# Kernel tuning notes

Measured on AMD Instinct MI355X. Metric: run time of the kernel, lower is better.

## Reference

```python
import jax, jax.numpy as jnp
import numpy as np

D_MODEL = 1024
NHEAD = 16
D_HEAD = D_MODEL // NHEAD
D_FF = 2 * D_MODEL
EPS = 1e-5


def setup_inputs() -> dict:
    key = jax.random.key(0)
    ks = jax.random.split(key, 12)
    s = 1.0 / np.sqrt(D_MODEL)
    x = jax.random.normal(ks[0], (4, 1024, D_MODEL), dtype=jnp.float32)
    # per-head projections stacked: [H, d_model, d_head] (x @ W layout)
    wq = jax.random.normal(ks[1], (NHEAD, D_MODEL, D_HEAD), dtype=jnp.float32) * s
    bq = jnp.zeros((NHEAD, D_HEAD), dtype=jnp.float32)
    wk = jax.random.normal(ks[2], (NHEAD, D_MODEL, D_HEAD), dtype=jnp.float32) * s
    bk = jnp.zeros((NHEAD, D_HEAD), dtype=jnp.float32)
    wv = jax.random.normal(ks[3], (NHEAD, D_MODEL, D_HEAD), dtype=jnp.float32) * s
    bv = jnp.zeros((NHEAD, D_HEAD), dtype=jnp.float32)
    wo_w = jax.random.normal(ks[4], (D_MODEL, D_MODEL), dtype=jnp.float32) * s
    wo_b = jnp.zeros((D_MODEL,), dtype=jnp.float32)
    ff1_w = jax.random.normal(ks[5], (D_MODEL, D_FF), dtype=jnp.float32) * s
    ff1_b = jnp.zeros((D_FF,), dtype=jnp.float32)
    ff2_w = jax.random.normal(ks[6], (D_FF, D_MODEL), dtype=jnp.float32) * (1.0 / np.sqrt(D_FF))
    ff2_b = jnp.zeros((D_MODEL,), dtype=jnp.float32)
    g1 = jnp.ones((D_MODEL,), dtype=jnp.float32)
    b1 = jnp.zeros((D_MODEL,), dtype=jnp.float32)
    g2 = jnp.ones((D_MODEL,), dtype=jnp.float32)
    b2 = jnp.zeros((D_MODEL,), dtype=jnp.float32)
    return dict(x=x, wq=wq, bq=bq, wk=wk, bk=bk, wv=wv, bv=bv,
                wo_w=wo_w, wo_b=wo_b, g1=g1, b1=b1,
                ff1_w=ff1_w, ff1_b=ff1_b, ff2_w=ff2_w, ff2_b=ff2_b,
                g2=g2, b2=b2)


def manual_layernorm(x, gamma, beta):
    # faithful to source: (x - mean) / (std + eps), std unbiased=False
    mean = jnp.mean(x, axis=-1, keepdims=True)
    std = jnp.sqrt(jnp.mean((x - mean) ** 2, axis=-1, keepdims=True))
    return gamma * (x - mean) / (std + EPS) + beta


def reference(x, wq, bq, wk, bk, wv, bv, wo_w, wo_b, g1, b1,
              ff1_w, ff1_b, ff2_w, ff2_b, g2, b2):
    B, S, D = x.shape
    # per-head projections, vectorized over heads: [B,H,S,d_head]
    q = jnp.einsum('bsd,hdk->bhsk', x, wq) + bq[None, :, None, :]
    k = jnp.einsum('bsd,hdk->bhsk', x, wk) + bk[None, :, None, :]
    v = jnp.einsum('bsd,hdk->bhsk', x, wv) + bv[None, :, None, :]
    scores = jnp.einsum('bhsk,bhtk->bhst', q, k) / jnp.sqrt(jnp.float32(D_HEAD))
    weights = jax.nn.softmax(scores, axis=-1)
    attn = jnp.einsum('bhst,bhtk->bhsk', weights, v)
    # concat heads back to [B,S,D]
    concat = jnp.transpose(attn, (0, 2, 1, 3)).reshape(B, S, D)
    proj = concat @ wo_w + wo_b
    h = manual_layernorm(x + proj, g1, b1)
    ff = jax.nn.relu(h @ ff1_w + ff1_b) @ ff2_w + ff2_b
    return manual_layernorm(h + ff, g2, b2)
```

## Files before the change

### kernel.cpp

```cpp
#include <hip/hip_runtime.h>
#include <hip/hip_bf16.h>

typedef __attribute__((ext_vector_type(8))) short bf16x8;
typedef __attribute__((ext_vector_type(4))) float f32x4;
using bf16 = __hip_bfloat16;

#define NTOK 4096
#define EPS_LN 1e-5f
#define QSCL 0.1803368801111244f

enum { EPI_F32 = 0, EPI_QKV = 1, EPI_RELU_BF16 = 2, EPI_BF16 = 3 };

#define VM8 asm volatile("s_waitcnt vmcnt(8)" ::: "memory")
#define VM0 asm volatile("s_waitcnt vmcnt(0)" ::: "memory")
#define LGKM0 asm volatile("s_waitcnt lgkmcnt(0)" ::: "memory")
#define SCHED0 __builtin_amdgcn_sched_barrier(0)
#define NOVM
#define DSRO(dst, ad, off) \
  asm volatile("ds_read_b128 %0, %1 offset:" #off : "=v"(dst) : "v"(ad))

__device__ inline void gload_lds16(const void* g, void* l) {
  __builtin_amdgcn_global_load_lds(
      (const __attribute__((address_space(1))) char*)g,
      (__attribute__((address_space(3))) char*)l, 16, 0, 0);
}

__device__ inline unsigned ldsoff(const void* p) {
  return (unsigned)(size_t)(const __attribute__((address_space(3))) char*)p;
}

__device__ inline unsigned short f2bfu(float x) {
  bf16 h = __float2bfloat16(x);
  return __builtin_bit_cast(unsigned short, h);
}
__device__ inline bf16 to_bf16(float v) { return __float2bfloat16(v); }
__device__ inline bf16 to_bf16(bf16 v) { return v; }

__device__ inline unsigned cvtpk(float lo, float hi) {
  unsigned r;
  asm volatile("v_cvt_pk_bf16_f32 %0, %1, %2" : "=v"(r) : "v"(lo), "v"(hi));
  return r;
}
__device__ inline float bu2f(unsigned short u) {
  unsigned v = (unsigned)u << 16;
  return __builtin_bit_cast(float, v);
}


__global__ __launch_bounds__(256) void cvt_bf16_kernel(const float* __restrict__ src,
                                                       bf16* __restrict__ dst, int n4) {
  int i = blockIdx.x * 256 + threadIdx.x;
  if (i >= n4) return;
  float4 v = ((const float4*)src)[i];
  ushort4 o;
  o.x = f2bfu(v.x); o.y = f2bfu(v.y); o.z = f2bfu(v.z); o.w = f2bfu(v.w);
  ((ushort4*)dst)[i] = o;
}

template <typename ST>
__global__ __launch_bounds__(256) void transpose_cvt(const ST* __restrict__ src,
                                                     bf16* __restrict__ dst, int R, int C) {
  __shared__ bf16 tile[32][33];
  int o = blockIdx.z;
  int r0 = blockIdx.y * 32, c0 = blockIdx.x * 32;
  int tx = threadIdx.x & 31, ty = threadIdx.x >> 5;
  const ST* s = src + (size_t)o * R * C;
  bf16* d = dst + (size_t)o * R * C;
#pragma unroll
  for (int i = 0; i < 32; i += 8)
    tile[ty + i][tx] = to_bf16(s[(size_t)(r0 + ty + i) * C + (c0 + tx)]);
  __syncthreads();
#pragma unroll
  for (int i = 0; i < 32; i += 8)
    d[(size_t)(c0 + ty + i) * R + (r0 + tx)] = tile[tx][ty + i];
}

__global__ __launch_bounds__(256) void pack_bias_kernel(const float* __restrict__ bq,
                                                        const float* __restrict__ bk,
                                                        const float* __restrict__ bv,
                                                        float* __restrict__ out) {
  int i = blockIdx.x * 256 + threadIdx.x;
  if (i >= 3072) return;
  out[i] = (i < 1024) ? bq[i] : (i < 2048 ? bk[i - 1024] : bv[i - 2048]);
}


#define STG(KOFF, DD) { _Pragma("unroll") for (int q = 0; q < 4; ++q) { \
    gload_lds16(gA0 + (KOFF) + (size_t)(q * 32) * lda2, \
                sAb + (DD) * 16384 + q * 4096 + w * 1024); \
    gload_lds16(gB0 + (KOFF) + (size_t)(q * 32) * ldb2, \
                sBb + (DD) * 16384 + q * 4096 + w * 1024); } }

#define TILE(OFFLIT, STG_, VMS) { \
  _Pragma("unroll") for (int i = 0; i < 4; ++i) { \
    DSRO(a[i][0], adA[i][0], OFFLIT); \
    DSRO(a[i][1], adA[i][1], OFFLIT); \
  } \
  _Pragma("unroll") for (int j = 0; j < 4; ++j) { \
    DSRO(b[j][0], adB[j][0], OFFLIT); \
    DSRO(b[j][1], adB[j][1], OFFLIT); \
  } \
  LGKM0; SCHED0; \
  __builtin_amdgcn_s_barrier(); \
  STG_; \
  __builtin_amdgcn_s_setprio(1); \
  _Pragma("unroll") for (int i = 0; i < 4; ++i) \
  _Pragma("unroll") for (int j = 0; j < 4; ++j) \
  _Pragma("unroll") for (int kk = 0; kk < 2; ++kk) \
    acc[i][j] = __builtin_amdgcn_mfma_f32_16x16x32_bf16( \
        a[i][kk], b[j][kk], acc[i][j], 0, 0, 0); \
  __builtin_amdgcn_s_setprio(0); \
  VMS; \
  __builtin_amdgcn_s_barrier(); }

__global__ __launch_bounds__(256, 2) void gemm128(
    const bf16* __restrict__ A, int lda,
    const bf16* __restrict__ Bt, int ldb,
    int M, int N, int K,
    int nbm, int nbn,
    const float* __restrict__ bias,
    float* __restrict__ Cf, bf16* __restrict__ Cb,
    bf16* __restrict__ Qd, bf16* __restrict__ Kd, bf16* __restrict__ Vd,
    int mode) {
  __shared__ bf16 sA[2][128][64];
  __shared__ bf16 sB[2][128][64];
  const int nwg = nbm * nbn;
  const int orig = blockIdx.x;
  const int wgid = (orig % 8) * (nwg / 8) + orig / 8;
  const int bm = wgid / nbn, bn = wgid % nbn;
  const int tid = threadIdx.x;
  const int w = tid >> 6, lane = tid & 63;
  const int wm = w >> 1, wn = w & 1;
  const int ri = lane & 15, kg = lane >> 4;
  const bf16* Ab = A + (size_t)bm * 128 * lda;
  const bf16* Bb = Bt + (size_t)bn * 128 * ldb;
  const int NT = K / 64;
  const size_t lda2 = (size_t)lda * 2, ldb2 = (size_t)ldb * 2;
  char* sAb = (char*)&sA[0][0][0];
  char* sBb = (char*)&sB[0][0][0];

  unsigned adA[4][2], adB[4][2];
  const unsigned sA0 = ldsoff(sAb), sB0 = ldsoff(sBb);
#pragma unroll
  for (int i = 0; i < 4; ++i) {
    int row = wm * 64 + i * 16 + ri;
    unsigned swz = (unsigned)((row & 7) << 4);
    adA[i][0] = sA0 + row * 128 + ((kg * 16) ^ swz);
    adA[i][1] = sA0 + row * 128 + ((64 + kg * 16) ^ swz);
  }
#pragma unroll
  for (int j = 0; j < 4; ++j) {
    int row = wn * 64 + j * 16 + ri;
    unsigned swz = (unsigned)((row & 7) << 4);
    adB[j][0] = sB0 + row * 128 + ((kg * 16) ^ swz);
    adB[j][1] = sB0 + row * 128 + ((64 + kg * 16) ^ swz);
  }

  const int r0 = tid >> 3;
  const int cb0 = ((tid & 7) * 16) ^ ((r0 & 7) << 4);
  const char* gA0 = (const char*)Ab + (size_t)r0 * lda2 + cb0;
  const char* gB0 = (const char*)Bb + (size_t)r0 * ldb2 + cb0;

  f32x4 acc[4][4] = {};
  bf16x8 a[4][2], b[4][2];

  STG(0, 0) STG(128, 1)
  VM8;
  __builtin_amdgcn_s_barrier();

  const int niter = NT / 2 - 1;
  for (int it = 0; it < niter; ++it) {
    TILE(0,     STG(256, 0), VM8)
    TILE(16384, STG(384, 1), VM8)
    gA0 += 256; gB0 += 256;
  }
  TILE(0,     , VM0)
  TILE(16384, , NOVM)

  const int colbase = bn * 128 + wn * 64 + ri;
  float bv4[4];
#pragma unroll
  for (int nf = 0; nf < 4; ++nf)
    bv4[nf] = bias ? bias[colbase + nf * 16] : 0.f;

  if (mode == EPI_QKV) {
    int col0 = bn * 128 + wn * 64;
    int which = col0 >> 10, hh = (col0 >> 6) & 15;
    bf16* dst = (which == 0) ? Qd : (which == 1) ? Kd : Vd;
    float scl = (which == 0) ? QSCL : 1.0f;
#pragma unroll
    for (int mf = 0; mf < 4; ++mf)
#pragma unroll
      for (int r = 0; r < 4; ++r) {
        int row = bm * 128 + wm * 64 + mf * 16 + kg * 4 + r;
        int b2 = row >> 10, s = row & 1023;
        bf16* o = dst + (((size_t)(b2 * 16 + hh)) * 1024 + s) * 64;
#pragma unroll
        for (int nf = 0; nf < 4; ++nf)
          o[nf * 16 + ri] = __float2bfloat16((acc[mf][nf][r] + bv4[nf]) * scl);
      }
  } else if (mode == EPI_F32) {
#pragma unroll
    for (int mf = 0; mf < 4; ++mf)
#pragma unroll
      for (int r = 0; r < 4; ++r) {
        int row = bm * 128 + wm * 64 + mf * 16 + kg * 4 + r;
        float* o = Cf + (size_t)row * N + colbase;
#pragma unroll
        for (int nf = 0; nf < 4; ++nf) o[nf * 16] = acc[mf][nf][r] + bv4[nf];
      }
  } else if (mode == EPI_RELU_BF16) {
#pragma unroll
    for (int mf = 0; mf < 4; ++mf)
#pragma unroll
      for (int r = 0; r < 4; ++r) {
        int row = bm * 128 + wm * 64 + mf * 16 + kg * 4 + r;
        bf16* o = Cb + (size_t)row * N + colbase;
#pragma unroll
        for (int nf = 0; nf < 4; ++nf) {
          float v = acc[mf][nf][r] + bv4[nf];
          o[nf * 16] = __float2bfloat16(v > 0.f ? v : 0.f);
        }
      }
  } else {
#pragma unroll
    for (int mf = 0; mf < 4; ++mf)
#pragma unroll
      for (int r = 0; r < 4; ++r) {
        int row = bm * 128 + wm * 64 + mf * 16 + kg * 4 + r;
        bf16* o = Cb + (size_t)row * N + colbase;
#pragma unroll
        for (int nf = 0; nf < 4; ++nf)
          o[nf * 16] = __float2bfloat16(acc[mf][nf][r] + bv4[nf]);
      }
  }
}

__global__ __launch_bounds__(256, 4) void attn_kernel(
    const bf16* __restrict__ Qb, const bf16* __restrict__ Kb,
    const bf16* __restrict__ Vs, bf16* __restrict__ Ob) {
  __shared__ bf16 KV[2][2][64][64];
  __shared__ bf16 Ps[4][16][64];
  const int orig = blockIdx.x;
  const int blk = (orig & 7) * 128 + (orig >> 3);
  const int bh = blk >> 4, qt = blk & 15;
  const int bb = bh >> 4, hh = bh & 15;
  const int tid = threadIdx.x, w = tid >> 6, lane = tid & 63;
  const int ri = lane & 15, kg = lane >> 4, r8 = lane >> 3;
  const int cb = ((lane & 7) * 16) ^ ((r8 & 7) << 4);
  const unsigned rsw = (unsigned)((ri & 7) << 4);
  const bf16* qp = Qb + (size_t)bh * 65536;
  const bf16* kp = Kb + (size_t)bh * 65536;
  const bf16* vp = Vs + (size_t)bh * 65536;
  const int q0 = qt * 64 + w * 16;
  const int c0 = w * 2, c1 = c0 + 1;

  unsigned offk0 = (unsigned)((kg * 16) ^ (int)rsw);
  unsigned offk1 = (unsigned)((64 + kg * 16) ^ (int)rsw);
  unsigned adF[4][2];
  const unsigned kv0 = ldsoff(&KV[0][0][0][0]);
#pragma unroll
  for (int n = 0; n < 4; ++n) {
    unsigned row = (unsigned)((n * 16 + ri) * 128);
    adF[n][0] = kv0 + row + offk0;
    adF[n][1] = kv0 + row + offk1;
  }
  const unsigned ps0 = ldsoff(&Ps[0][0][0]) + (unsigned)(w * 2048 + ri * 128);
  unsigned adPr[2] = {ps0 + offk0, ps0 + offk1};
  char* pwb = (char*)&Ps[0][0][0] + w * 2048 + ri * 128;
  char* adPw[4];
#pragma unroll
  for (int n = 0; n < 4; ++n)
    adPw[n] = pwb + ((n * 32 + kg * 8) ^ (int)rsw);

  bf16x8 qf[2];
  qf[0] = *(const bf16x8*)(qp + (size_t)(q0 + ri) * 64 + kg * 8);
  qf[1] = *(const bf16x8*)(qp + (size_t)(q0 + ri) * 64 + 32 + kg * 8);

  bf16x8 ones;
#pragma unroll
  for (int e = 0; e < 8; ++e) ones[e] = (short)0x3F80;

  f32x4 oacc[4] = {};
  f32x4 lacc = {};
  float mrun = -1e30f;

#define ASTAGE(T, D) { \
    gload_lds16((const char*)(kp + (size_t)((T) * 64 + c0 * 8 + r8) * 64) + cb, \
                (char*)KV + (D) * 16384 + c0 * 1024); \
    gload_lds16((const char*)(kp + (size_t)((T) * 64 + c1 * 8 + r8) * 64) + cb, \
                (char*)KV + (D) * 16384 + c1 * 1024); \
    gload_lds16((const char*)(vp + (size_t)(c0 * 8 + r8) * 1024 + (T) * 64) + cb, \
                (char*)KV + (D) * 16384 + 8192 + c0 * 1024); \
    gload_lds16((const char*)(vp + (size_t)(c1 * 8 + r8) * 1024 + (T) * 64) + cb, \
                (char*)KV + (D) * 16384 + 8192 + c1 * 1024); }

#define ATILE(KOFF, VOFF, STG_, ENDSYNC) { \
  bf16x8 kf0[4], kf1[4]; \
  _Pragma("unroll") for (int n = 0; n < 4; ++n) { \
    DSRO(kf0[n], adF[n][0], KOFF); \
    DSRO(kf1[n], adF[n][1], KOFF); \
  } \
  STG_; \
  LGKM0; SCHED0; \
  f32x4 sac[4] = {}; \
  _Pragma("unroll") for (int n = 0; n < 4; ++n) { \
    sac[n] = __builtin_amdgcn_mfma_f32_16x16x32_bf16(kf0[n], qf[0], sac[n], 0, 0, 0); \
    sac[n] = __builtin_amdgcn_mfma_f32_16x16x32_bf16(kf1[n], qf[1], sac[n], 0, 0, 0); \
  } \
  float mx[4]; \
  _Pragma("unroll") for (int n = 0; n < 4; ++n) \
    mx[n] = fmaxf(fmaxf(sac[n][0], sac[n][1]), fmaxf(sac[n][2], sac[n][3])); \
  float mt16 = fmaxf(fmaxf(mx[0], mx[1]), fmaxf(mx[2], mx[3])); \
  if (!__all(mt16 - mrun <= 8.f)) { \
    float mrow = fmaxf(mt16, __shfl_xor(mt16, 16)); \
    mrow = fmaxf(mrow, __shfl_xor(mrow, 32)); \
    float mnew = fmaxf(mrun, mrow); \
    float corr = exp2f(mrun - mnew); \
    mrun = mnew; \
    float cr[4]; \
    _Pragma("unroll") for (int r = 0; r < 4; ++r) cr[r] = __shfl(corr, kg * 4 + r); \
    _Pragma("unroll") for (int n = 0; n < 4; ++n) { \
      oacc[n][0] *= cr[0]; oacc[n][1] *= cr[1]; \
      oacc[n][2] *= cr[2]; oacc[n][3] *= cr[3]; \
    } \
    lacc[0] *= cr[0]; lacc[1] *= cr[1]; lacc[2] *= cr[2]; lacc[3] *= cr[3]; \
  } \
  _Pragma("unroll") for (int n = 0; n < 4; ++n) { \
    uint2 pk; \
    pk.x = cvtpk(exp2f(sac[n][0] - mrun), exp2f(sac[n][1] - mrun)); \
    pk.y = cvtpk(exp2f(sac[n][2] - mrun), exp2f(sac[n][3] - mrun)); \
    *(uint2*)adPw[n] = pk; \
  } \
  LGKM0; \
  bf16x8 pf0, pf1, vf0[4], vf1[4]; \
  DSRO(pf0, adPr[0], 0); \
  DSRO(pf1, adPr[1], 0); \
  _Pragma("unroll") for (int n = 0; n < 4; ++n) { \
    DSRO(vf0[n], adF[n][0], VOFF); \
    DSRO(vf1[n], adF[n][1], VOFF); \
  } \
  LGKM0; SCHED0; \
  _Pragma("unroll") for (int n = 0; n < 4; ++n) { \
    oacc[n] = __builtin_amdgcn_mfma_f32_16x16x32_bf16(pf0, vf0[n], oacc[n], 0, 0, 0); \
    oacc[n] = __builtin_amdgcn_mfma_f32_16x16x32_bf16(pf1, vf1[n], oacc[n], 0, 0, 0); \
  } \
  lacc = __builtin_amdgcn_mfma_f32_16x16x32_bf16(pf0, ones, lacc, 0, 0, 0); \
  lacc = __builtin_amdgcn_mfma_f32_16x16x32_bf16(pf1, ones, lacc, 0, 0, 0); \
  ENDSYNC }

#define SYNCT { VM0; __syncthreads(); }

  ASTAGE(0, 0);
  VM0;
  __syncthreads();

  for (int tt = 0; tt < 7; ++tt) {
    const int t2 = tt * 2;
    ATILE(0,     8192,  ASTAGE(t2 + 1, 1), SYNCT)
    ATILE(16384, 24576, ASTAGE(t2 + 2, 0), SYNCT)
  }
  ATILE(0,     8192,  ASTAGE(15, 1), SYNCT)
  ATILE(16384, 24576, ,              )

  float ivr[4];
#pragma unroll
  for (int r = 0; r < 4; ++r) ivr[r] = 1.f / lacc[r];
#pragma unroll
  for (int r = 0; r < 4; ++r) {
    int s = q0 + kg * 4 + r;
    size_t base = ((size_t)(bb * 1024 + s)) * 1024 + hh * 64;
#pragma unroll
    for (int n = 0; n < 4; ++n)
      Ob[base + n * 16 + ri] = __float2bfloat16(oacc[n][r] * ivr[r]);
  }
#undef ASTAGE
#undef ATILE
#undef SYNCT
}

__global__ __launch_bounds__(256) void ln_bb(
    const bf16* __restrict__ a, const bf16* __restrict__ b,
    const float* __restrict__ gamma, const float* __restrict__ beta,
    float* __restrict__ out_f32, bf16* __restrict__ out_bf16) {
  int row = blockIdx.x;
  int tid = threadIdx.x;
  ushort4 au = ((const ushort4*)(a + (size_t)row * 1024))[tid];
  ushort4 bu = ((const ushort4*)(b + (size_t)row * 1024))[tid];
  float4 z;
  z.x = bu2f(au.x) + bu2f(bu.x);
  z.y = bu2f(au.y) + bu2f(bu.y);
  z.z = bu2f(au.z) + bu2f(bu.z);
  z.w = bu2f(au.w) + bu2f(bu.w);
  float s = z.x + z.y + z.z + z.w;
  float ss = z.x * z.x + z.y * z.y + z.z * z.z + z.w * z.w;
#pragma unroll
  for (int o = 32; o >= 1; o >>= 1) { s += __shfl_xor(s, o); ss += __shfl_xor(ss, o); }
  __shared__ float red[8];
  int wid = tid >> 6;
  if ((tid & 63) == 0) { red[wid] = s; red[4 + wid] = ss; }
  __syncthreads();
  s = red[0] + red[1] + red[2] + red[3];
  ss = red[4] + red[5] + red[6] + red[7];
  float mean = s * (1.f / 1024.f);
  float var = ss * (1.f / 1024.f) - mean * mean;
  var = var > 0.f ? var : 0.f;
  float inv = 1.f / (sqrtf(var) + EPS_LN);
  float4 g = ((const float4*)gamma)[tid];
  float4 be = ((const float4*)beta)[tid];
  float4 y;
  y.x = (z.x - mean) * inv * g.x + be.x;
  y.y = (z.y - mean) * inv * g.y + be.y;
  y.z = (z.z - mean) * inv * g.z + be.z;
  y.w = (z.w - mean) * inv * g.w + be.w;
  ((float4*)(out_f32 + (size_t)row * 1024))[tid] = y;
  ushort4 o;
  o.x = f2bfu(y.x); o.y = f2bfu(y.y); o.z = f2bfu(y.z); o.w = f2bfu(y.w);
  ((ushort4*)(out_bf16 + (size_t)row * 1024))[tid] = o;
}

__global__ __launch_bounds__(256) void ln_fb(
    const float* __restrict__ a, const bf16* __restrict__ b,
    const float* __restrict__ gamma, const float* __restrict__ beta,
    float* __restrict__ out_f32) {
  int row = blockIdx.x;
  int tid = threadIdx.x;
  float4 av = ((const float4*)(a + (size_t)row * 1024))[tid];
  ushort4 bu = ((const ushort4*)(b + (size_t)row * 1024))[tid];
  float4 z;
  z.x = av.x + bu2f(bu.x);
  z.y = av.y + bu2f(bu.y);
  z.z = av.z + bu2f(bu.z);
  z.w = av.w + bu2f(bu.w);
  float s = z.x + z.y + z.z + z.w;
  float ss = z.x * z.x + z.y * z.y + z.z * z.z + z.w * z.w;
#pragma unroll
  for (int o = 32; o >= 1; o >>= 1) { s += __shfl_xor(s, o); ss += __shfl_xor(ss, o); }
  __shared__ float red[8];
  int wid = tid >> 6;
  if ((tid & 63) == 0) { red[wid] = s; red[4 + wid] = ss; }
  __syncthreads();
  s = red[0] + red[1] + red[2] + red[3];
  ss = red[4] + red[5] + red[6] + red[7];
  float mean = s * (1.f / 1024.f);
  float var = ss * (1.f / 1024.f) - mean * mean;
  var = var > 0.f ? var : 0.f;
  float inv = 1.f / (sqrtf(var) + EPS_LN);
  float4 g = ((const float4*)gamma)[tid];
  float4 be = ((const float4*)beta)[tid];
  float4 y;
  y.x = (z.x - mean) * inv * g.x + be.x;
  y.y = (z.y - mean) * inv * g.y + be.y;
  y.z = (z.z - mean) * inv * g.z + be.z;
  y.w = (z.w - mean) * inv * g.w + be.w;
  ((float4*)(out_f32 + (size_t)row * 1024))[tid] = y;
}

extern "C" void kernel_launch(void* const* d_in, const int* in_sizes, int n_in,
                              void* d_out, int out_size, void* d_ws, size_t ws_size,
                              hipStream_t stream) {
  const float* x = (const float*)d_in[0];
  const float* wq = (const float*)d_in[1];
  const float* bq = (const float*)d_in[2];
  const float* wk = (const float*)d_in[3];
  const float* bk = (const float*)d_in[4];
  const float* wv = (const float*)d_in[5];
  const float* bv = (const float*)d_in[6];
  const float* wo_w = (const float*)d_in[7];
  const float* wo_b = (const float*)d_in[8];
  const float* g1 = (const float*)d_in[9];
  const float* b1 = (const float*)d_in[10];
  const float* ff1w = (const float*)d_in[11];
  const float* ff1b = (const float*)d_in[12];
  const float* ff2w = (const float*)d_in[13];
  const float* ff2b = (const float*)d_in[14];
  const float* g2 = (const float*)d_in[15];
  const float* b2 = (const float*)d_in[16];

  char* ws = (char*)d_ws;
  size_t off = 0;
  auto alloc = [&](size_t bytes) {
    char* p = ws + off;
    off += (bytes + 255) & ~(size_t)255;
    return p;
  };
  bf16* xb = (bf16*)alloc((size_t)NTOK * 1024 * 2);
  bf16* wqkvt = (bf16*)alloc((size_t)3072 * 1024 * 2);
  bf16* wot = (bf16*)alloc((size_t)1024 * 1024 * 2);
  bf16* ff1t = (bf16*)alloc((size_t)2048 * 1024 * 2);
  bf16* ff2t = (bf16*)alloc((size_t)1024 * 2048 * 2);
  float* qkvbias = (float*)alloc(3072 * 4);
  bf16* qbuf = (bf16*)alloc((size_t)64 * 1024 * 64 * 2);
  bf16* kbuf = (bf16*)alloc((size_t)64 * 1024 * 64 * 2);
  bf16* vbuf = (bf16*)alloc((size_t)64 * 1024 * 64 * 2);
  bf16* vtb = (bf16*)alloc((size_t)64 * 64 * 1024 * 2);
  bf16* attnb = (bf16*)alloc((size_t)NTOK * 1024 * 2);
  bf16* projb = (bf16*)alloc((size_t)NTOK * 1024 * 2);
  bf16* hb = (bf16*)alloc((size_t)NTOK * 1024 * 2);
  bf16* ff1o = qbuf;
  float* hbuf = (float*)d_out;

  cvt_bf16_kernel<<<(NTOK * 1024 / 4 + 255) / 256, 256, 0, stream>>>(x, xb, NTOK * 1024 / 4);
  transpose_cvt<float><<<dim3(2, 32, 16), 256, 0, stream>>>(wq, wqkvt, 1024, 64);
  transpose_cvt<float><<<dim3(2, 32, 16), 256, 0, stream>>>(wk, wqkvt + 1024 * 1024, 1024, 64);
  transpose_cvt<float><<<dim3(2, 32, 16), 256, 0, stream>>>(wv, wqkvt + 2 * 1024 * 1024, 1024, 64);
  transpose_cvt<float><<<dim3(32, 32, 1), 256, 0, stream>>>(wo_w, wot, 1024, 1024);
  transpose_cvt<float><<<dim3(64, 32, 1), 256, 0, stream>>>(ff1w, ff1t, 1024, 2048);
  transpose_cvt<float><<<dim3(32, 64, 1), 256, 0, stream>>>(ff2w, ff2t, 2048, 1024);
  pack_bias_kernel<<<12, 256, 0, stream>>>(bq, bk, bv, qkvbias);

  gemm128<<<768, 256, 0, stream>>>(xb, 1024, wqkvt, 1024, 4096, 3072, 1024,
                                   32, 24, qkvbias,
                                   nullptr, nullptr, qbuf, kbuf, vbuf, EPI_QKV);
  transpose_cvt<bf16><<<dim3(2, 32, 64), 256, 0, stream>>>(vbuf, vtb, 1024, 64);
  attn_kernel<<<dim3(1024), 256, 0, stream>>>(qbuf, kbuf, vtb, attnb);
  gemm128<<<256, 256, 0, stream>>>(attnb, 1024, wot, 1024, 4096, 1024, 1024,
                                   32, 8, wo_b,
                                   nullptr, projb, nullptr, nullptr, nullptr, EPI_BF16);
  ln_bb<<<4096, 256, 0, stream>>>(xb, projb, g1, b1, hbuf, hb);
  gemm128<<<512, 256, 0, stream>>>(hb, 1024, ff1t, 1024, 4096, 2048, 1024,
                                   32, 16, ff1b,
                                   nullptr, ff1o, nullptr, nullptr, nullptr, EPI_RELU_BF16);
  gemm128<<<256, 256, 0, stream>>>(ff1o, 2048, ff2t, 2048, 4096, 1024, 2048,
                                   32, 8, ff2b,
                                   nullptr, projb, nullptr, nullptr, nullptr, EPI_BF16);
  ln_fb<<<4096, 256, 0, stream>>>(hbuf, projb, g2, b2, (float*)d_out);
}
```

Before: 167.3 us.

## Add 128x192 QKV GEMM and 128x64 GEMMs for N=1024 layers, drop fp32 residual

```diff
diff --git a/kernel.cpp b/kernel.cpp
--- a/kernel.cpp
+++ b/kernel.cpp
@@ -11,7 +11,9 @@
 
 enum { EPI_F32 = 0, EPI_QKV = 1, EPI_RELU_BF16 = 2, EPI_BF16 = 3 };
 
+#define VM10 asm volatile("s_waitcnt vmcnt(10)" ::: "memory")
 #define VM8 asm volatile("s_waitcnt vmcnt(8)" ::: "memory")
+#define VM6 asm volatile("s_waitcnt vmcnt(6)" ::: "memory")
 #define VM0 asm volatile("s_waitcnt vmcnt(0)" ::: "memory")
 #define LGKM0 asm volatile("s_waitcnt lgkmcnt(0)" ::: "memory")
 #define SCHED0 __builtin_amdgcn_sched_barrier(0)
@@ -84,6 +86,226 @@
   out[i] = (i < 1024) ? bq[i] : (i < 2048 ? bk[i - 1024] : bv[i - 2048]);
 }
 
+
+#define STG192(KOFF, DD) { \
+  _Pragma("unroll") for (int q = 0; q < 4; ++q) \
+    gload_lds16(gA0 + (KOFF) + (size_t)(q * 32) * lda2, \
+                sAb + (DD) * 16384 + q * 4096 + w * 1024); \
+  _Pragma("unroll") for (int q = 0; q < 6; ++q) \
+    gload_lds16(gB0 + (KOFF) + (size_t)(q * 32) * ldb2, \
+                sBb + (DD) * 24576 + q * 4096 + w * 1024); }
+
+#define TILE192(AOFF, BOFF, STG_, VMS) { \
+  _Pragma("unroll") for (int i = 0; i < 4; ++i) { \
+    DSRO(a[i][0], adA[i][0], AOFF); \
+    DSRO(a[i][1], adA[i][1], AOFF); \
+  } \
+  _Pragma("unroll") for (int j = 0; j < 6; ++j) { \
+    DSRO(b[j][0], adB[j][0], BOFF); \
+    DSRO(b[j][1], adB[j][1], BOFF); \
+  } \
+  LGKM0; SCHED0; \
+  __builtin_amdgcn_s_barrier(); \
+  STG_; \
+  __builtin_amdgcn_s_setprio(1); \
+  _Pragma("unroll") for (int i = 0; i < 4; ++i) \
+  _Pragma("unroll") for (int j = 0; j < 6; ++j) \
+  _Pragma("unroll") for (int kk = 0; kk < 2; ++kk) \
+    acc[i][j] = __builtin_amdgcn_mfma_f32_16x16x32_bf16( \
+        a[i][kk], b[j][kk], acc[i][j], 0, 0, 0); \
+  __builtin_amdgcn_s_setprio(0); \
+  VMS; \
+  __builtin_amdgcn_s_barrier(); }
+
+__global__ __launch_bounds__(256, 2) void gemm192(
+    const bf16* __restrict__ A, int lda,
+    const bf16* __restrict__ Bt, int ldb, int K,
+    int nbm, int nbn,
+    const float* __restrict__ bias,
+    bf16* __restrict__ Qd, bf16* __restrict__ Kd, bf16* __restrict__ Vd) {
+  __shared__ bf16 sA[2][128][64];
+  __shared__ bf16 sB[2][192][64];
+  const int nwg = nbm * nbn;
+  const int orig = blockIdx.x;
+  const int wgid = (orig % 8) * (nwg / 8) + orig / 8;
+  const int bm = wgid / nbn, bn = wgid % nbn;
+  const int tid = threadIdx.x;
+  const int w = tid >> 6, lane = tid & 63;
+  const int wm = w >> 1, wn = w & 1;
+  const int ri = lane & 15, kg = lane >> 4;
+  const bf16* Ab = A + (size_t)bm * 128 * lda;
+  const bf16* Bb = Bt + (size_t)bn * 192 * ldb;
+  const int NT = K / 64;
+  const size_t lda2 = (size_t)lda * 2, ldb2 = (size_t)ldb * 2;
+  char* sAb = (char*)&sA[0][0][0];
+  char* sBb = (char*)&sB[0][0][0];
+
+  unsigned adA[4][2], adB[6][2];
+  const unsigned sA0 = ldsoff(sAb), sB0 = ldsoff(sBb);
+#pragma unroll
+  for (int i = 0; i < 4; ++i) {
+    int row = wm * 64 + i * 16 + ri;
+    unsigned swz = (unsigned)((row & 7) << 4);
+    adA[i][0] = sA0 + row * 128 + ((kg * 16) ^ swz);
+    adA[i][1] = sA0 + row * 128 + ((64 + kg * 16) ^ swz);
+  }
+#pragma unroll
+  for (int j = 0; j < 6; ++j) {
+    int row = wn * 96 + j * 16 + ri;
+    unsigned swz = (unsigned)((row & 7) << 4);
+    adB[j][0] = sB0 + row * 128 + ((kg * 16) ^ swz);
+    adB[j][1] = sB0 + row * 128 + ((64 + kg * 16) ^ swz);
+  }
+
+  const int r0 = tid >> 3;
+  const int cb0 = ((tid & 7) * 16) ^ ((r0 & 7) << 4);
+  const char* gA0 = (const char*)Ab + (size_t)r0 * lda2 + cb0;
+  const char* gB0 = (const char*)Bb + (size_t)r0 * ldb2 + cb0;
+
+  f32x4 acc[4][6] = {};
+  bf16x8 a[4][2], b[6][2];
+
+  STG192(0, 0) STG192(128, 1)
+  VM10;
+  __builtin_amdgcn_s_barrier();
+
+  const int niter = NT / 2 - 1;
+  for (int it = 0; it < niter; ++it) {
+    TILE192(0,     0,     STG192(256, 0), VM10)
+    TILE192(16384, 24576, STG192(384, 1), VM10)
+    gA0 += 256; gB0 += 256;
+  }
+  TILE192(0,     0,     , VM0)
+  TILE192(16384, 24576, , NOVM)
+
+#pragma unroll
+  for (int nf = 0; nf < 6; ++nf) {
+    int col0 = bn * 192 + wn * 96 + nf * 16;
+    int which = col0 >> 10;
+    int hh = (col0 >> 6) & 15;
+    int dk0 = col0 & 63;
+    bf16* dst = (which == 0) ? Qd : (which == 1) ? Kd : Vd;
+    float scl = (which == 0) ? QSCL : 1.0f;
+    float bv = bias[col0 + ri];
+#pragma unroll
+    for (int mf = 0; mf < 4; ++mf)
+#pragma unroll
+      for (int r = 0; r < 4; ++r) {
+        int row = bm * 128 + wm * 64 + mf * 16 + kg * 4 + r;
+        int b2 = row >> 10, s = row & 1023;
+        dst[(((size_t)(b2 * 16 + hh)) * 1024 + s) * 64 + dk0 + ri] =
+            __float2bfloat16((acc[mf][nf][r] + bv) * scl);
+      }
+  }
+}
+
+
+#define STG64(KOFF, DD) { \
+  _Pragma("unroll") for (int q = 0; q < 4; ++q) \
+    gload_lds16(gA0 + (KOFF) + (size_t)(q * 32) * lda2, \
+                sAb + (DD) * 16384 + q * 4096 + w * 1024); \
+  _Pragma("unroll") for (int q = 0; q < 2; ++q) \
+    gload_lds16(gB0 + (KOFF) + (size_t)(q * 32) * ldb2, \
+                sBb + (DD) * 8192 + q * 4096 + w * 1024); }
+
+#define TILE64(AOFF, BOFF, STG_, VMS) { \
+  _Pragma("unroll") for (int i = 0; i < 4; ++i) { \
+    DSRO(a[i][0], adA[i][0], AOFF); \
+    DSRO(a[i][1], adA[i][1], AOFF); \
+  } \
+  _Pragma("unroll") for (int j = 0; j < 2; ++j) { \
+    DSRO(b[j][0], adB[j][0], BOFF); \
+    DSRO(b[j][1], adB[j][1], BOFF); \
+  } \
+  LGKM0; SCHED0; \
+  __builtin_amdgcn_s_barrier(); \
+  STG_; \
+  __builtin_amdgcn_s_setprio(1); \
+  _Pragma("unroll") for (int i = 0; i < 4; ++i) \
+  _Pragma("unroll") for (int j = 0; j < 2; ++j) \
+  _Pragma("unroll") for (int kk = 0; kk < 2; ++kk) \
+    acc[i][j] = __builtin_amdgcn_mfma_f32_16x16x32_bf16( \
+        a[i][kk], b[j][kk], acc[i][j], 0, 0, 0); \
+  __builtin_amdgcn_s_setprio(0); \
+  VMS; \
+  __builtin_amdgcn_s_barrier(); }
+
+__global__ __launch_bounds__(256, 3) void gemm64(
+    const bf16* __restrict__ A, int lda,
+    const bf16* __restrict__ Bt, int ldb,
+    int N, int K, int nbm, int nbn,
+    const float* __restrict__ bias,
+    bf16* __restrict__ Cb) {
+  __shared__ bf16 sA[2][128][64];
+  __shared__ bf16 sB[2][64][64];
+  const int nwg = nbm * nbn;
+  const int orig = blockIdx.x;
+  const int wgid = (orig % 8) * (nwg / 8) + orig / 8;
+  const int bm = wgid / nbn, bn = wgid % nbn;
+  const int tid = threadIdx.x;
+  const int w = tid >> 6, lane = tid & 63;
+  const int wm = w >> 1, wn = w & 1;
+  const int ri = lane & 15, kg = lane >> 4;
+  const bf16* Ab = A + (size_t)bm * 128 * lda;
+  const bf16* Bb = Bt + (size_t)bn * 64 * ldb;
+  const int NT = K / 64;
+  const size_t lda2 = (size_t)lda * 2, ldb2 = (size_t)ldb * 2;
+  char* sAb = (char*)&sA[0][0][0];
+  char* sBb = (char*)&sB[0][0][0];
+
+  unsigned adA[4][2], adB[2][2];
+  const unsigned sA0 = ldsoff(sAb), sB0 = ldsoff(sBb);
+#pragma unroll
+  for (int i = 0; i < 4; ++i) {
+    int row = wm * 64 + i * 16 + ri;
+    unsigned swz = (unsigned)((row & 7) << 4);
+    adA[i][0] = sA0 + row * 128 + ((kg * 16) ^ swz);
+    adA[i][1] = sA0 + row * 128 + ((64 + kg * 16) ^ swz);
+  }
+#pragma unroll
+  for (int j = 0; j < 2; ++j) {
+    int row = wn * 32 + j * 16 + ri;
+    unsigned swz = (unsigned)((row & 7) << 4);
+    adB[j][0] = sB0 + row * 128 + ((kg * 16) ^ swz);
+    adB[j][1] = sB0 + row * 128 + ((64 + kg * 16) ^ swz);
+  }
+
+  const int r0 = tid >> 3;
+  const int cb0 = ((tid & 7) * 16) ^ ((r0 & 7) << 4);
+  const char* gA0 = (const char*)Ab + (size_t)r0 * lda2 + cb0;
+  const char* gB0 = (const char*)Bb + (size_t)r0 * ldb2 + cb0;
+
+  f32x4 acc[4][2] = {};
+  bf16x8 a[4][2], b[2][2];
+
+  STG64(0, 0) STG64(128, 1)
+  VM6;
+  __builtin_amdgcn_s_barrier();
+
+  const int niter = NT / 2 - 1;
+  for (int it = 0; it < niter; ++it) {
+    TILE64(0,     0,    STG64(256, 0), VM6)
+    TILE64(16384, 8192, STG64(384, 1), VM6)
+    gA0 += 256; gB0 += 256;
+  }
+  TILE64(0,     0,    , VM0)
+  TILE64(16384, 8192, , NOVM)
+
+  const int colbase = bn * 64 + wn * 32 + ri;
+  float bv2[2];
+#pragma unroll
+  for (int nf = 0; nf < 2; ++nf) bv2[nf] = bias[colbase + nf * 16];
+#pragma unroll
+  for (int mf = 0; mf < 4; ++mf)
+#pragma unroll
+    for (int r = 0; r < 4; ++r) {
+      int row = bm * 128 + wm * 64 + mf * 16 + kg * 4 + r;
+      bf16* o = Cb + (size_t)row * N + colbase;
+#pragma unroll
+      for (int nf = 0; nf < 2; ++nf)
+        o[nf * 16] = __float2bfloat16(acc[mf][nf][r] + bv2[nf]);
+    }
+}
 
 #define STG(KOFF, DD) { _Pragma("unroll") for (int q = 0; q < 4; ++q) { \
     gload_lds16(gA0 + (KOFF) + (size_t)(q * 32) * lda2, \
@@ -116,12 +338,9 @@
 __global__ __launch_bounds__(256, 2) void gemm128(
     const bf16* __restrict__ A, int lda,
     const bf16* __restrict__ Bt, int ldb,
-    int M, int N, int K,
-    int nbm, int nbn,
+    int N, int K, int nbm, int nbn,
     const float* __restrict__ bias,
-    float* __restrict__ Cf, bf16* __restrict__ Cb,
-    bf16* __restrict__ Qd, bf16* __restrict__ Kd, bf16* __restrict__ Vd,
-    int mode) {
+    bf16* __restrict__ Cb) {
   __shared__ bf16 sA[2][128][64];
   __shared__ bf16 sB[2][128][64];
   const int nwg = nbm * nbn;
@@ -180,60 +399,19 @@
   const int colbase = bn * 128 + wn * 64 + ri;
   float bv4[4];
 #pragma unroll
-  for (int nf = 0; nf < 4; ++nf)
-    bv4[nf] = bias ? bias[colbase + nf * 16] : 0.f;
-
-  if (mode == EPI_QKV) {
-    int col0 = bn * 128 + wn * 64;
-    int which = col0 >> 10, hh = (col0 >> 6) & 15;
-    bf16* dst = (which == 0) ? Qd : (which == 1) ? Kd : Vd;
-    float scl = (which == 0) ? QSCL : 1.0f;
-#pragma unroll
-    for (int mf = 0; mf < 4; ++mf)
-#pragma unroll
-      for (int r = 0; r < 4; ++r) {
-        int row = bm * 128 + wm * 64 + mf * 16 + kg * 4 + r;
-        int b2 = row >> 10, s = row & 1023;
-        bf16* o = dst + (((size_t)(b2 * 16 + hh)) * 1024 + s) * 64;
-#pragma unroll
-        for (int nf = 0; nf < 4; ++nf)
-          o[nf * 16 + ri] = __float2bfloat16((acc[mf][nf][r] + bv4[nf]) * scl);
+  for (int nf = 0; nf < 4; ++nf) bv4[nf] = bias[colbase + nf * 16];
+#pragma unroll
+  for (int mf = 0; mf < 4; ++mf)
+#pragma unroll
+    for (int r = 0; r < 4; ++r) {
+      int row = bm * 128 + wm * 64 + mf * 16 + kg * 4 + r;
+      bf16* o = Cb + (size_t)row * N + colbase;
+#pragma unroll
+      for (int nf = 0; nf < 4; ++nf) {
+        float v = acc[mf][nf][r] + bv4[nf];
+        o[nf * 16] = __float2bfloat16(v > 0.f ? v : 0.f);
       }
-  } else if (mode == EPI_F32) {
-#pragma unroll
-    for (int mf = 0; mf < 4; ++mf)
-#pragma unroll
-      for (int r = 0; r < 4; ++r) {
-        int row = bm * 128 + wm * 64 + mf * 16 + kg * 4 + r;
-        float* o = Cf + (size_t)row * N + colbase;
-#pragma unroll
-        for (int nf = 0; nf < 4; ++nf) o[nf * 16] = acc[mf][nf][r] + bv4[nf];
-      }
-  } else if (mode == EPI_RELU_BF16) {
-#pragma unroll
-    for (int mf = 0; mf < 4; ++mf)
-#pragma unroll
-      for (int r = 0; r < 4; ++r) {
-        int row = bm * 128 + wm * 64 + mf * 16 + kg * 4 + r;
-        bf16* o = Cb + (size_t)row * N + colbase;
-#pragma unroll
-        for (int nf = 0; nf < 4; ++nf) {
-          float v = acc[mf][nf][r] + bv4[nf];
-          o[nf * 16] = __float2bfloat16(v > 0.f ? v : 0.f);
-        }
-      }
-  } else {
-#pragma unroll
-    for (int mf = 0; mf < 4; ++mf)
-#pragma unroll
-      for (int r = 0; r < 4; ++r) {
-        int row = bm * 128 + wm * 64 + mf * 16 + kg * 4 + r;
-        bf16* o = Cb + (size_t)row * N + colbase;
-#pragma unroll
-        for (int nf = 0; nf < 4; ++nf)
-          o[nf * 16] = __float2bfloat16(acc[mf][nf][r] + bv4[nf]);
-      }
-  }
+    }
 }
 
 __global__ __launch_bounds__(256, 4) void attn_kernel(
@@ -413,47 +591,13 @@
   y.y = (z.y - mean) * inv * g.y + be.y;
   y.z = (z.z - mean) * inv * g.z + be.z;
   y.w = (z.w - mean) * inv * g.w + be.w;
-  ((float4*)(out_f32 + (size_t)row * 1024))[tid] = y;
-  ushort4 o;
-  o.x = f2bfu(y.x); o.y = f2bfu(y.y); o.z = f2bfu(y.z); o.w = f2bfu(y.w);
-  ((ushort4*)(out_bf16 + (size_t)row * 1024))[tid] = o;
-}
-
-__global__ __launch_bounds__(256) void ln_fb(
-    const float* __restrict__ a, const bf16* __restrict__ b,
-    const float* __restrict__ gamma, const float* __restrict__ beta,
-    float* __restrict__ out_f32) {
-  int row = blockIdx.x;
-  int tid = threadIdx.x;
-  float4 av = ((const float4*)(a + (size_t)row * 1024))[tid];
-  ushort4 bu = ((const ushort4*)(b + (size_t)row * 1024))[tid];
-  float4 z;
-  z.x = av.x + bu2f(bu.x);
-  z.y = av.y + bu2f(bu.y);
-  z.z = av.z + bu2f(bu.z);
-  z.w = av.w + bu2f(bu.w);
-  float s = z.x + z.y + z.z + z.w;
-  float ss = z.x * z.x + z.y * z.y + z.z * z.z + z.w * z.w;
-#pragma unroll
-  for (int o = 32; o >= 1; o >>= 1) { s += __shfl_xor(s, o); ss += __shfl_xor(ss, o); }
-  __shared__ float red[8];
-  int wid = tid >> 6;
-  if ((tid & 63) == 0) { red[wid] = s; red[4 + wid] = ss; }
-  __syncthreads();
-  s = red[0] + red[1] + red[2] + red[3];
-  ss = red[4] + red[5] + red[6] + red[7];
-  float mean = s * (1.f / 1024.f);
-  float var = ss * (1.f / 1024.f) - mean * mean;
-  var = var > 0.f ? var : 0.f;
-  float inv = 1.f / (sqrtf(var) + EPS_LN);
-  float4 g = ((const float4*)gamma)[tid];
-  float4 be = ((const float4*)beta)[tid];
-  float4 y;
-  y.x = (z.x - mean) * inv * g.x + be.x;
-  y.y = (z.y - mean) * inv * g.y + be.y;
-  y.z = (z.z - mean) * inv * g.z + be.z;
-  y.w = (z.w - mean) * inv * g.w + be.w;
-  ((float4*)(out_f32 + (size_t)row * 1024))[tid] = y;
+  if (out_f32)
+    ((float4*)(out_f32 + (size_t)row * 1024))[tid] = y;
+  if (out_bf16) {
+    ushort4 o;
+    o.x = f2bfu(y.x); o.y = f2bfu(y.y); o.z = f2bfu(y.z); o.w = f2bfu(y.w);
+    ((ushort4*)(out_bf16 + (size_t)row * 1024))[tid] = o;
+  }
 }
 
 extern "C" void kernel_launch(void* const* d_in, const int* in_sizes, int n_in,
@@ -498,7 +642,6 @@
   bf16* projb = (bf16*)alloc((size_t)NTOK * 1024 * 2);
   bf16* hb = (bf16*)alloc((size_t)NTOK * 1024 * 2);
   bf16* ff1o = qbuf;
-  float* hbuf = (float*)d_out;
 
   cvt_bf16_kernel<<<(NTOK * 1024 / 4 + 255) / 256, 256, 0, stream>>>(x, xb, NTOK * 1024 / 4);
   transpose_cvt<float><<<dim3(2, 32, 16), 256, 0, stream>>>(wq, wqkvt, 1024, 64);
@@ -509,20 +652,16 @@
   transpose_cvt<float><<<dim3(32, 64, 1), 256, 0, stream>>>(ff2w, ff2t, 2048, 1024);
   pack_bias_kernel<<<12, 256, 0, stream>>>(bq, bk, bv, qkvbias);
 
-  gemm128<<<768, 256, 0, stream>>>(xb, 1024, wqkvt, 1024, 4096, 3072, 1024,
-                                   32, 24, qkvbias,
-                                   nullptr, nullptr, qbuf, kbuf, vbuf, EPI_QKV);
+  gemm192<<<512, 256, 0, stream>>>(xb, 1024, wqkvt, 1024, 1024, 32, 16, qkvbias,
+                                   qbuf, kbuf, vbuf);
   transpose_cvt<bf16><<<dim3(2, 32, 64), 256, 0, stream>>>(vbuf, vtb, 1024, 64);
   attn_kernel<<<dim3(1024), 256, 0, stream>>>(qbuf, kbuf, vtb, attnb);
-  gemm128<<<256, 256, 0, stream>>>(attnb, 1024, wot, 1024, 4096, 1024, 1024,
-                                   32, 8, wo_b,
-                                   nullptr, projb, nullptr, nullptr, nullptr, EPI_BF16);
-  ln_bb<<<4096, 256, 0, stream>>>(xb, projb, g1, b1, hbuf, hb);
-  gemm128<<<512, 256, 0, stream>>>(hb, 1024, ff1t, 1024, 4096, 2048, 1024,
-                                   32, 16, ff1b,
-                                   nullptr, ff1o, nullptr, nullptr, nullptr, EPI_RELU_BF16);
-  gemm128<<<256, 256, 0, stream>>>(ff1o, 2048, ff2t, 2048, 4096, 1024, 2048,
-                                   32, 8, ff2b,
-                                   nullptr, projb, nullptr, nullptr, nullptr, EPI_BF16);
-  ln_fb<<<4096, 256, 0, stream>>>(hbuf, projb, g2, b2, (float*)d_out);
-}
+  gemm64<<<512, 256, 0, stream>>>(attnb, 1024, wot, 1024, 1024, 1024, 32, 16,
+                                  wo_b, projb);
+  ln_bb<<<4096, 256, 0, stream>>>(xb, projb, g1, b1, nullptr, hb);
+  gemm128<<<512, 256, 0, stream>>>(hb, 1024, ff1t, 1024, 2048, 1024, 32, 16,
+                                   ff1b, ff1o);
+  gemm64<<<512, 256, 0, stream>>>(ff1o, 2048, ff2t, 2048, 1024, 2048, 32, 16,
+                                  ff2b, projb);
+  ln_bb<<<4096, 256, 0, stream>>>(hb, projb, g2, b2, (float*)d_out, nullptr);
+}
```

Result: faster. 158.3 us (-5.4%).
